# Kernel optimization log

Hardware: AMD Instinct MI355X
Metric: run time of the kernel (lower is better)

Reference implementation:

```python
import jax, jax.numpy as jnp
import numpy as np

N = 10000
F_IN = 512
HID = 256
C = 16
N_POST_ITER = 4


def setup_inputs() -> dict:
    key = jax.random.key(0)
    ks = jax.random.split(key, 10)
    raw_adj = jax.random.uniform(ks[0], (N, N), dtype=jnp.float32) * 0.01
    A = jax.random.uniform(ks[1], (N, N), dtype=jnp.float32)
    normed_adj = A / jnp.sum(A, axis=1, keepdims=True)  # row-sum-one normalized
    features = jax.random.normal(ks[2], (N, F_IN), dtype=jnp.float32)
    labels = jax.random.randint(ks[3], (N,), 0, C)
    y_onehot = jax.nn.one_hot(labels, C, dtype=jnp.float32)
    train_mask = jax.random.randint(ks[4], (N,), 0, 2).astype(jnp.bool_)
    # GCN belief estimator params (glorot-ish scaling)
    W1 = jax.random.normal(ks[5], (F_IN, HID), dtype=jnp.float32) / np.sqrt(F_IN)
    b1 = jnp.zeros((HID,), dtype=jnp.float32)
    W2 = jax.random.normal(ks[6], (HID, C), dtype=jnp.float32) / np.sqrt(HID)
    b2 = jnp.zeros((C,), dtype=jnp.float32)
    # class-compatibility matrix H (initialized, zero-centered as in init_H)
    H = jax.random.normal(ks[7], (C, C), dtype=jnp.float32) * 0.1
    return {"raw_adj": raw_adj, "normed_adj": normed_adj, "features": features,
            "y_onehot": y_onehot, "train_mask": train_mask,
            "W1": W1, "b1": b1, "W2": W2, "b2": b2, "H": H}


def reference(raw_adj, normed_adj, features, y_onehot, train_mask, W1, b1, W2, b2, H):
    num_class = y_onehot.shape[1]
    # 2-layer GCN belief estimator: adj @ (x @ W) + b
    h = jax.nn.relu(normed_adj @ (features @ W1) + b1)          # [N, HID]
    logits = normed_adj @ (h @ W2) + b2                          # [N, C]
    # post_process: iterative compatibility-guided belief propagation
    prior_belief = jax.nn.softmax(logits, axis=1)
    E_hat = prior_belief - 1.0 / num_class
    B_hat = E_hat
    for _ in range(N_POST_ITER):
        B_hat = E_hat + raw_adj @ (B_hat @ H)
    post_belief = B_hat + 1.0 / num_class
    return post_belief
```

## Files before the change

kernel.cpp:

```cpp
#include <hip/hip_runtime.h>

#define NN 10000
#define KP 10048
static constexpr float INV_C = 1.0f / 16.0f;

typedef __attribute__((ext_vector_type(8))) short bf16x8;
typedef __attribute__((ext_vector_type(4))) float f32x4;
typedef unsigned short u16;
typedef unsigned int u32;

__device__ __forceinline__ u16 f2b(float f) {
    union { float f; u32 u; } v; v.f = f;
    u32 r = v.u + 0x7FFFu + ((v.u >> 16) & 1u);
    return (u16)(r >> 16);
}
__device__ __forceinline__ float b2f(u16 b) {
    union { u32 u; float f; } v; v.u = ((u32)b) << 16;
    return v.f;
}

#define AS1(p) ((__attribute__((address_space(1))) void*)(p))
#define AS3(p) ((__attribute__((address_space(3))) void*)(p))
#define NTL4(p)  __builtin_nontemporal_load((const f32x4*)(p))
#define NTL8H(p) __builtin_nontemporal_load((const bf16x8*)(p))

__global__ __launch_bounds__(256)
void cvt_feat(const float* __restrict__ src, u16* __restrict__ dst)
{
    int c = blockIdx.x * 256 + threadIdx.x;
    size_t base = (size_t)c * 8;
    f32x4 a = NTL4(src + base);
    f32x4 b = NTL4(src + base + 4);
    bf16x8 o;
    o[0]=f2b(a[0]); o[1]=f2b(a[1]); o[2]=f2b(a[2]); o[3]=f2b(a[3]);
    o[4]=f2b(b[0]); o[5]=f2b(b[1]); o[6]=f2b(b[2]); o[7]=f2b(b[3]);
    *(bf16x8*)(dst + base) = o;
}

__global__ __launch_bounds__(256)
void w12t(const float* __restrict__ W1, const float* __restrict__ W2,
          float* __restrict__ W1T, u16* __restrict__ W2T)
{
    int bid = blockIdx.x, t = threadIdx.x;
    if (bid < 512) {
        int idx = bid * 256 + t;
        int n = idx >> 9, k = idx & 511;
        W1T[idx] = W1[(size_t)k * 256 + n];
    } else {
        int idx = (bid - 512) * 256 + t;
        if (idx < 4096) {
            int n_ = idx >> 8, k_ = idx & 255;
            W2T[idx] = f2b(W2[(size_t)k_ * 16 + n_]);
        }
    }
}

template<int BIAS, int RELU>
__global__ __launch_bounds__(256)
void gemm_a32_bt16(const float* __restrict__ A, int lda, int M, int Ka,
                   const u16* __restrict__ BT, int ldb, int N, int npad,
                   const float* __restrict__ bias,
                   u16* __restrict__ C, int ldc, int K)
{
    __shared__ u16 Asm[64 * 64];
    __shared__ u16 Bsm[256 * 64];
    const int t = threadIdx.x;
    const int lane = t & 63;
    const int w = t >> 6;
    const int row0 = blockIdx.x * 64;
    const int n0 = blockIdx.y * 256;

    const f32x4 fz = {0.f, 0.f, 0.f, 0.f};
    f32x4 acc[4][4];
#pragma unroll
    for (int i = 0; i < 4; ++i)
#pragma unroll
        for (int j = 0; j < 4; ++j) acc[i][j] = fz;

    const int ar = t >> 2, akq = t & 3;
    int agr = row0 + ar; if (agr > M - 1) agr = M - 1;
    const float* asrc = A + (size_t)agr * lda + akq * 16;
    const int aslot0 = (akq * 2) ^ (ar & 7);
    const int aslot1 = (akq * 2 + 1) ^ (ar & 7);
    const int l8 = lane >> 3, sl = lane & 7;

    for (int k0 = 0; k0 < K; k0 += 64) {
#pragma unroll
        for (int i = 0; i < 8; ++i) {
            int lr = i * 32 + w * 8 + l8;
            int gn = n0 + lr; if (gn > N - 1) gn = N - 1;
            int ss = sl ^ (lr & 7);
            const u16* src = BT + (size_t)gn * ldb + k0 + ss * 8;
            __builtin_amdgcn_global_load_lds(AS1(src), AS3(&Bsm[(i * 32 + w * 8) * 64]),
                                             16, 0, 0);
        }
        bool aval = (k0 + akq * 16) < Ka;
        f32x4 x0, x1, x2, x3;
        if (aval) {
            x0 = *(const f32x4*)(asrc + k0);
            x1 = *(const f32x4*)(asrc + k0 + 4);
            x2 = *(const f32x4*)(asrc + k0 + 8);
            x3 = *(const f32x4*)(asrc + k0 + 12);
        } else {
            x0 = x1 = x2 = x3 = fz;
        }
        bf16x8 p0, p1;
        p0[0]=f2b(x0[0]); p0[1]=f2b(x0[1]); p0[2]=f2b(x0[2]); p0[3]=f2b(x0[3]);
        p0[4]=f2b(x1[0]); p0[5]=f2b(x1[1]); p0[6]=f2b(x1[2]); p0[7]=f2b(x1[3]);
        p1[0]=f2b(x2[0]); p1[1]=f2b(x2[1]); p1[2]=f2b(x2[2]); p1[3]=f2b(x2[3]);
        p1[4]=f2b(x3[0]); p1[5]=f2b(x3[1]); p1[6]=f2b(x3[2]); p1[7]=f2b(x3[3]);
        *(bf16x8*)&Asm[ar * 64 + aslot0 * 8] = p0;
        *(bf16x8*)&Asm[ar * 64 + aslot1 * 8] = p1;
        __syncthreads();
#pragma unroll
        for (int kk = 0; kk < 2; ++kk) {
            bf16x8 afr[4], bfr[4];
#pragma unroll
            for (int mi = 0; mi < 4; ++mi) {
                int r = mi * 16 + (lane & 15);
                int s2 = (kk * 4 + (lane >> 4)) ^ (r & 7);
                afr[mi] = *(const bf16x8*)&Asm[r * 64 + s2 * 8];
            }
#pragma unroll
            for (int ni = 0; ni < 4; ++ni) {
                int nr = w * 64 + ni * 16 + (lane & 15);
                int s2 = (kk * 4 + (lane >> 4)) ^ (nr & 7);
                bfr[ni] = *(const bf16x8*)&Bsm[nr * 64 + s2 * 8];
            }
#pragma unroll
            for (int mi = 0; mi < 4; ++mi)
#pragma unroll
                for (int ni = 0; ni < 4; ++ni)
                    acc[mi][ni] = __builtin_amdgcn_mfma_f32_16x16x32_bf16(
                        afr[mi], bfr[ni], acc[mi][ni], 0, 0, 0);
        }
        __syncthreads();
    }
#pragma unroll
    for (int mi = 0; mi < 4; ++mi) {
        int grb = row0 + mi * 16 + (lane >> 4) * 4;
#pragma unroll
        for (int ni = 0; ni < 4; ++ni) {
            int gc = n0 + w * 64 + ni * 16 + (lane & 15);
            if (gc < npad) {
                float bv = (BIAS && gc < N) ? bias[gc] : 0.f;
#pragma unroll
                for (int rg = 0; rg < 4; ++rg) {
                    int gr = grb + rg;
                    if (gr < M) {
                        float v = acc[mi][ni][rg] + bv;
                        if (RELU) v = fmaxf(v, 0.f);
                        C[(size_t)gr * ldc + gc] = f2b(gc < N ? v : 0.f);
                    }
                }
            }
        }
    }
}

template<int CVT>
__global__ __launch_bounds__(256)
void gemm_na(const float* __restrict__ A, const u16* __restrict__ BT,
             u16* __restrict__ Pws, u16* __restrict__ Acvt)
{
    __shared__ u16 Asm[64 * 64];
    __shared__ u16 Bsm[256 * 64];
    const int t = threadIdx.x;
    const int lane = t & 63;
    const int w = t >> 6;
    const int row0 = blockIdx.x * 64;
    const int s = blockIdx.y;
    const int c0 = (157 * s) >> 3, c1 = (157 * (s + 1)) >> 3;

    const f32x4 fz = {0.f, 0.f, 0.f, 0.f};
    f32x4 acc[4][4];
#pragma unroll
    for (int i = 0; i < 4; ++i)
#pragma unroll
        for (int j = 0; j < 4; ++j) acc[i][j] = fz;

    const int ar = t >> 2, akq = t & 3;
    const int grow = row0 + ar;
    const int agr = grow < NN ? grow : NN - 1;
    const float* asrc = A + (size_t)agr * NN + akq * 16;
    const int aslot0 = (akq * 2) ^ (ar & 7);
    const int aslot1 = (akq * 2 + 1) ^ (ar & 7);
    const int l8 = lane >> 3, sl = lane & 7;

    for (int ck = c0; ck < c1; ++ck) {
        const int k0 = ck * 64;
#pragma unroll
        for (int i = 0; i < 8; ++i) {
            int lr = i * 32 + w * 8 + l8;
            int ss = sl ^ (lr & 7);
            const u16* src = BT + (size_t)lr * KP + k0 + ss * 8;
            __builtin_amdgcn_global_load_lds(AS1(src), AS3(&Bsm[(i * 32 + w * 8) * 64]),
                                             16, 0, 0);
        }
        const int kq0 = k0 + akq * 16;
        bool aval = kq0 < NN;
        f32x4 x0, x1, x2, x3;
        if (aval) {
            x0 = NTL4(asrc + k0);
            x1 = NTL4(asrc + k0 + 4);
            x2 = NTL4(asrc + k0 + 8);
            x3 = NTL4(asrc + k0 + 12);
        } else {
            x0 = x1 = x2 = x3 = fz;
        }
        bf16x8 p0, p1;
        p0[0]=f2b(x0[0]); p0[1]=f2b(x0[1]); p0[2]=f2b(x0[2]); p0[3]=f2b(x0[3]);
        p0[4]=f2b(x1[0]); p0[5]=f2b(x1[1]); p0[6]=f2b(x1[2]); p0[7]=f2b(x1[3]);
        p1[0]=f2b(x2[0]); p1[1]=f2b(x2[1]); p1[2]=f2b(x2[2]); p1[3]=f2b(x2[3]);
        p1[4]=f2b(x3[0]); p1[5]=f2b(x3[1]); p1[6]=f2b(x3[2]); p1[7]=f2b(x3[3]);
        *(bf16x8*)&Asm[ar * 64 + aslot0 * 8] = p0;
        *(bf16x8*)&Asm[ar * 64 + aslot1 * 8] = p1;
        if (CVT && grow < NN) {
            *(bf16x8*)(Acvt + (size_t)grow * KP + kq0) = p0;
            *(bf16x8*)(Acvt + (size_t)grow * KP + kq0 + 8) = p1;
        }
        __syncthreads();
#pragma unroll
        for (int kk = 0; kk < 2; ++kk) {
            bf16x8 afr[4], bfr[4];
#pragma unroll
            for (int mi = 0; mi < 4; ++mi) {
                int r = mi * 16 + (lane & 15);
                int s2 = (kk * 4 + (lane >> 4)) ^ (r & 7);
                afr[mi] = *(const bf16x8*)&Asm[r * 64 + s2 * 8];
            }
#pragma unroll
            for (int ni = 0; ni < 4; ++ni) {
                int nr = w * 64 + ni * 16 + (lane & 15);
                int s2 = (kk * 4 + (lane >> 4)) ^ (nr & 7);
                bfr[ni] = *(const bf16x8*)&Bsm[nr * 64 + s2 * 8];
            }
#pragma unroll
            for (int mi = 0; mi < 4; ++mi)
#pragma unroll
                for (int ni = 0; ni < 4; ++ni)
                    acc[mi][ni] = __builtin_amdgcn_mfma_f32_16x16x32_bf16(
                        afr[mi], bfr[ni], acc[mi][ni], 0, 0, 0);
        }
        __syncthreads();
    }
    u16* outp = Pws + (size_t)s * NN * 256;
#pragma unroll
    for (int mi = 0; mi < 4; ++mi) {
        int grb = row0 + mi * 16 + (lane >> 4) * 4;
#pragma unroll
        for (int ni = 0; ni < 4; ++ni) {
            int gc = w * 64 + ni * 16 + (lane & 15);
#pragma unroll
            for (int rg = 0; rg < 4; ++rg) {
                int gr = grb + rg;
                if (gr < NN)
                    outp[(size_t)gr * 256 + gc] = f2b(acc[mi][ni][rg]);
            }
        }
    }
}

__global__ __launch_bounds__(256)
void reduce_h(const u16* __restrict__ Pws, const float* __restrict__ b1,
              u16* __restrict__ hbf)
{
    int i8 = blockIdx.x * 256 + threadIdx.x;
    size_t base = (size_t)i8 * 8;
    int col = (int)(base & 255);
    float v[8];
#pragma unroll
    for (int j = 0; j < 8; ++j) v[j] = b1[col + j];
#pragma unroll
    for (int s = 0; s < 8; ++s) {
        bf16x8 p = NTL8H(Pws + (size_t)s * NN * 256 + base);
#pragma unroll
        for (int j = 0; j < 8; ++j) v[j] += b2f((u16)p[j]);
    }
    bf16x8 o;
#pragma unroll
    for (int j = 0; j < 8; ++j) o[j] = f2b(fmaxf(v[j], 0.f));
    *(bf16x8*)(hbf + base) = o;
}

template<int AFP32, int CVT, int NTA16>
__global__ __launch_bounds__(256)
void adj16(const void* __restrict__ Av, long lda,
           const u16* __restrict__ BT,
           float* __restrict__ Pout, int nch, int nchf,
           u16* __restrict__ Acvt)
{
    const int t = threadIdx.x, lane = t & 63, w = t >> 6;
    const int s = blockIdx.y;
    const int rowu = blockIdx.x * 64 + w * 16 + (lane & 15);
    const int row = rowu < NN ? rowu : NN - 1;
    const int kq = (lane >> 4) * 8;
    const u16* brow = BT + (size_t)(lane & 15) * KP + kq;
    const float* a32 = (const float*)Av + (size_t)row * lda + kq;
    const u16*  a16 = (const u16*) Av + (size_t)row * lda + kq;
    u16* cvtp = CVT ? (Acvt + (size_t)rowu * KP + kq) : (u16*)0;
    const bool wok = CVT && (rowu < NN);

    int c0 = (nch * s) >> 3, c1 = (nch * (s + 1)) >> 3;
    int c1f = c1 < nchf ? c1 : nchf;
    f32x4 acc = {0.f, 0.f, 0.f, 0.f};
    int kc = c0;
    for (; kc + 4 <= c1f; kc += 4) {
        bf16x8 a[4], b[4];
#pragma unroll
        for (int u = 0; u < 4; ++u) {
            if (AFP32) {
                f32x4 x = NTL4(a32 + (size_t)(kc + u) * 32);
                f32x4 y = NTL4(a32 + (size_t)(kc + u) * 32 + 4);
                bf16x8 r;
                r[0]=f2b(x[0]); r[1]=f2b(x[1]); r[2]=f2b(x[2]); r[3]=f2b(x[3]);
                r[4]=f2b(y[0]); r[5]=f2b(y[1]); r[6]=f2b(y[2]); r[7]=f2b(y[3]);
                a[u] = r;
            } else if (NTA16) {
                a[u] = NTL8H(a16 + (size_t)(kc + u) * 32);
            } else {
                a[u] = *(const bf16x8*)(a16 + (size_t)(kc + u) * 32);
            }
            b[u] = *(const bf16x8*)(brow + (size_t)(kc + u) * 32);
        }
        if (CVT && wok) {
#pragma unroll
            for (int u = 0; u < 4; ++u)
                *(bf16x8*)(cvtp + (size_t)(kc + u) * 32) = a[u];
        }
#pragma unroll
        for (int u = 0; u < 4; ++u)
            acc = __builtin_amdgcn_mfma_f32_16x16x32_bf16(a[u], b[u], acc, 0, 0, 0);
    }
    for (; kc < c1; ++kc) {
        bf16x8 a = bf16x8{0,0,0,0,0,0,0,0};
        if (AFP32) {
            if (kc * 32 + kq < NN) {
                f32x4 x = NTL4(a32 + (size_t)kc * 32);
                f32x4 y = NTL4(a32 + (size_t)kc * 32 + 4);
                a[0]=f2b(x[0]); a[1]=f2b(x[1]); a[2]=f2b(x[2]); a[3]=f2b(x[3]);
                a[4]=f2b(y[0]); a[5]=f2b(y[1]); a[6]=f2b(y[2]); a[7]=f2b(y[3]);
            }
        } else {
            a = *(const bf16x8*)(a16 + (size_t)kc * 32);
        }
        if (CVT && wok)
            *(bf16x8*)(cvtp + (size_t)kc * 32) = a;
        bf16x8 b = *(const bf16x8*)(brow + (size_t)kc * 32);
        acc = __builtin_amdgcn_mfma_f32_16x16x32_bf16(a, b, acc, 0, 0, 0);
    }
    int ob = blockIdx.x * 64 + w * 16 + (lane >> 4) * 4;
#pragma unroll
    for (int rg = 0; rg < 4; ++rg) {
        int orow = ob + rg;
        if (orow < NN)
            Pout[(size_t)s * (NN * 16) + (size_t)orow * 16 + (lane & 15)] = acc[rg];
    }
}

__global__ __launch_bounds__(256)
void hw2_mfma(const u16* __restrict__ h, const u16* __restrict__ W2T,
              u16* __restrict__ outT)
{
    const int t = threadIdx.x, lane = t & 63, w = t >> 6;
    int row = blockIdx.x * 64 + w * 16 + (lane & 15);
    int rowc = row < NN ? row : NN - 1;
    const int kq = (lane >> 4) * 8;
    const u16* arow = h + (size_t)rowc * 256 + kq;
    const u16* brow = W2T + (size_t)(lane & 15) * 256 + kq;
    f32x4 acc = {0.f, 0.f, 0.f, 0.f};
#pragma unroll
    for (int kc = 0; kc < 8; ++kc) {
        bf16x8 a = *(const bf16x8*)(arow + kc * 32);
        bf16x8 b = *(const bf16x8*)(brow + kc * 32);
        acc = __builtin_amdgcn_mfma_f32_16x16x32_bf16(a, b, acc, 0, 0, 0);
    }
    int ob = blockIdx.x * 64 + w * 16 + (lane >> 4) * 4;
    int col = lane & 15;
#pragma unroll
    for (int rg = 0; rg < 4; ++rg) {
        int r = ob + rg;
        outT[(size_t)col * KP + r] = f2b(r < NN ? acc[rg] : 0.f);
    }
}

__global__ __launch_bounds__(256)
void softmax_e_h2(const float* __restrict__ P, const float* __restrict__ b2,
                  const float* __restrict__ H, float* __restrict__ E,
                  u16* __restrict__ bhT)
{
    __shared__ float Hs[256];
    const int t = threadIdx.x;
    Hs[t] = H[t];
    __syncthreads();
    const int l = t & 63, w = t >> 6;
    const int g = l >> 2, sub = l & 3;
    const int row = blockIdx.x * 64 + w * 16 + g;
    const bool valid = row < NN;
    float acc[16];
#pragma unroll
    for (int k = 0; k < 16; ++k) acc[k] = 0.f;
    if (valid) {
        const float* p0 = P + (size_t)(sub * 2) * (NN * 16) + (size_t)row * 16;
        const float* p1 = p0 + (size_t)NN * 16;
#pragma unroll
        for (int q = 0; q < 4; ++q) {
            f32x4 a = *(const f32x4*)(p0 + q * 4);
            f32x4 c = *(const f32x4*)(p1 + q * 4);
#pragma unroll
            for (int j = 0; j < 4; ++j) acc[q * 4 + j] = a[j] + c[j];
        }
        if (sub == 0) {
#pragma unroll
            for (int k = 0; k < 16; ++k) acc[k] += b2[k];
        }
    }
#pragma unroll
    for (int m = 1; m <= 2; m <<= 1)
#pragma unroll
        for (int k = 0; k < 16; ++k) acc[k] += __shfl_xor(acc[k], m, 4);
    float e[16];
    if (valid) {
        float mx = acc[0];
#pragma unroll
        for (int k = 1; k < 16; ++k) mx = fmaxf(mx, acc[k]);
        float ssum = 0.f;
#pragma unroll
        for (int k = 0; k < 16; ++k) { e[k] = __expf(acc[k] - mx); ssum += e[k]; }
        float inv = 1.f / ssum;
#pragma unroll
        for (int k = 0; k < 16; ++k) e[k] = e[k] * inv - INV_C;
        f32x4 eq = {e[sub*4+0], e[sub*4+1], e[sub*4+2], e[sub*4+3]};
        *(f32x4*)(E + (size_t)row * 16 + sub * 4) = eq;
    } else {
#pragma unroll
        for (int k = 0; k < 16; ++k) e[k] = 0.f;
    }
    float o[4] = {0.f, 0.f, 0.f, 0.f};
#pragma unroll
    for (int m2 = 0; m2 < 16; ++m2) {
        float x = e[m2];
#pragma unroll
        for (int j = 0; j < 4; ++j) o[j] += x * Hs[m2 * 16 + sub * 4 + j];
    }
#pragma unroll
    for (int j = 0; j < 4; ++j)
        bhT[(size_t)(sub * 4 + j) * KP + row] = f2b(o[j]);
}

template<int LAST>
__global__ __launch_bounds__(256)
void combine_bmm2(const float* __restrict__ E, const float* __restrict__ P,
                  const float* __restrict__ H, u16* __restrict__ bhT,
                  float* __restrict__ out)
{
    __shared__ float Hs[256];
    const int t = threadIdx.x;
    Hs[t] = H[t];
    __syncthreads();
    const int l = t & 63, w = t >> 6;
    const int g = l >> 2, sub = l & 3;
    const int row = blockIdx.x * 64 + w * 16 + g;
    const bool valid = row < NN;
    float acc[16];
#pragma unroll
    for (int k = 0; k < 16; ++k) acc[k] = 0.f;
    if (valid) {
        const float* p0 = P + (size_t)(sub * 2) * (NN * 16) + (size_t)row * 16;
        const float* p1 = p0 + (size_t)NN * 16;
#pragma unroll
        for (int q = 0; q < 4; ++q) {
            f32x4 a = *(const f32x4*)(p0 + q * 4);
            f32x4 c = *(const f32x4*)(p1 + q * 4);
#pragma unroll
            for (int j = 0; j < 4; ++j) acc[q * 4 + j] = a[j] + c[j];
        }
        if (sub == 0) {
            const float* ep = E + (size_t)row * 16;
#pragma unroll
            for (int k = 0; k < 16; ++k) acc[k] += ep[k];
        }
    }
#pragma unroll
    for (int m = 1; m <= 2; m <<= 1)
#pragma unroll
        for (int k = 0; k < 16; ++k) acc[k] += __shfl_xor(acc[k], m, 4);
    if (LAST) {
        if (valid) {
            f32x4 oq = {acc[sub*4+0] + INV_C, acc[sub*4+1] + INV_C,
                        acc[sub*4+2] + INV_C, acc[sub*4+3] + INV_C};
            *(f32x4*)(out + (size_t)row * 16 + sub * 4) = oq;
        }
    } else {
        if (!valid) {
#pragma unroll
            for (int k = 0; k < 16; ++k) acc[k] = 0.f;
        }
        float o[4] = {0.f, 0.f, 0.f, 0.f};
#pragma unroll
        for (int m2 = 0; m2 < 16; ++m2) {
            float x = acc[m2];
#pragma unroll
            for (int j = 0; j < 4; ++j) o[j] += x * Hs[m2 * 16 + sub * 4 + j];
        }
#pragma unroll
        for (int j = 0; j < 4; ++j)
            bhT[(size_t)(sub * 4 + j) * KP + row] = f2b(o[j]);
    }
}

extern "C" void kernel_launch(void* const* d_in, const int* in_sizes, int n_in,
                              void* d_out, int out_size, void* d_ws, size_t ws_size,
                              hipStream_t stream)
{
    const float* raw_adj    = (const float*)d_in[0];
    const float* normed_adj = (const float*)d_in[1];
    const float* features   = (const float*)d_in[2];
    const float* W1 = (const float*)d_in[5];
    const float* b1 = (const float*)d_in[6];
    const float* W2 = (const float*)d_in[7];
    const float* b2 = (const float*)d_in[8];
    const float* H  = (const float*)d_in[9];
    float* out = (float*)d_out;

    char* ws = (char*)d_ws;
    u16*   featbf = (u16*)  (ws + 0);
    float* P      = (float*)(ws + 0);
    float* E      = (float*)(ws + 5120000);
    float* W1T    = (float*)(ws + 10240000);
    u16*   W2T    = (u16*)  (ws + 10764288);
    u16*   XWT    = (u16*)  (ws + 10772480);
    u16*   hbf    = (u16*)  (ws + 15917056);
    u16*   hw2T   = (u16*)  (ws + 21037056);
    u16*   bhT    = (u16*)  (ws + 21358592);
    const bool full = ws_size >= (size_t)263600128;
    const bool mid  = ws_size >= (size_t)222640128;
    const bool low  = ws_size >= (size_t)62640128;
    u16* An_bf = (u16*)(ws + 21680128);
    u16* ArBf  = (u16*)(ws + 21680128);
    u16* Pws   = (u16*)(ws + (full ? 222640128 : 21680128));

    cvt_feat<<<2500, 256, 0, stream>>>(features, featbf);
    w12t<<<528, 256, 0, stream>>>(W1, W2, W1T, W2T);

    gemm_a32_bt16<0, 0><<<dim3(4, 40), 256, 0, stream>>>(
        W1T, 512, 256, 512, featbf, 512, NN, KP, nullptr, XWT, KP, 512);

    if (low) {
        if (full)
            gemm_na<1><<<dim3(157, 8), 256, 0, stream>>>(normed_adj, XWT, Pws, An_bf);
        else
            gemm_na<0><<<dim3(157, 8), 256, 0, stream>>>(normed_adj, XWT, Pws, nullptr);
        reduce_h<<<1250, 256, 0, stream>>>(Pws, b1, hbf);
    } else {
        gemm_a32_bt16<1, 1><<<dim3(157, 1), 256, 0, stream>>>(
            normed_adj, NN, NN, NN, XWT, KP, 256, 256, b1, hbf, 256, KP);
    }

    hw2_mfma<<<157, 256, 0, stream>>>(hbf, W2T, hw2T);

    if (full)
        adj16<0, 0, 1><<<dim3(157, 8), 256, 0, stream>>>(
            (const void*)An_bf, KP, hw2T, P, 314, 314, nullptr);
    else
        adj16<1, 0, 0><<<dim3(157, 8), 256, 0, stream>>>(
            (const void*)normed_adj, NN, hw2T, P, 313, 312, nullptr);

    softmax_e_h2<<<157, 256, 0, stream>>>(P, b2, H, E, bhT);

    for (int it = 0; it < 4; ++it) {
        if (mid) {
            if (it == 0)
                adj16<1, 1, 0><<<dim3(157, 8), 256, 0, stream>>>(
                    (const void*)raw_adj, NN, bhT, P, 314, 312, ArBf);
            else
                adj16<0, 0, 0><<<dim3(157, 8), 256, 0, stream>>>(
                    (const void*)ArBf, KP, bhT, P, 314, 314, nullptr);
        } else {
            adj16<1, 0, 0><<<dim3(157, 8), 256, 0, stream>>>(
                (const void*)raw_adj, NN, bhT, P, 313, 312, nullptr);
        }
        if (it == 3)
            combine_bmm2<1><<<157, 256, 0, stream>>>(E, P, H, nullptr, out);
        else
            combine_bmm2<0><<<157, 256, 0, stream>>>(E, P, H, bhT, nullptr);
    }
}
```

Measured before the change: 670.0 us.

## Split normed_adj GEMM into 16 K-slices, drop nontemporal loads, dual accumulators

Doubles the K-split of the first adjacency GEMM from 8 to 16 slices, giving more blocks, and has reduce_h sum 16 partial buffers. The workspace thresholds grow to fit the larger partial buffer. All nontemporal loads become ordinary loads. The bf16 conversion now uses the library intrinsic, the A loads are issued before the B LDS loads, and adj16 splits its MFMA chain across two accumulators to shorten the dependency chain. The trade-offs are more partial-sum traffic, and the larger workspace requirement may push execution onto a slower fallback path.

New measurement: 605.3 us. -9.7%, faster.

```diff
diff --git a/kernel.cpp b/kernel.cpp
--- a/kernel.cpp
+++ b/kernel.cpp
@@ -1,4 +1,5 @@
 #include <hip/hip_runtime.h>
+#include <hip/hip_bf16.h>
 
 #define NN 10000
 #define KP 10048
@@ -10,31 +11,30 @@
 typedef unsigned int u32;
 
 __device__ __forceinline__ u16 f2b(float f) {
-    union { float f; u32 u; } v; v.f = f;
-    u32 r = v.u + 0x7FFFu + ((v.u >> 16) & 1u);
-    return (u16)(r >> 16);
+    return __builtin_bit_cast(u16, __float2bfloat16(f));
 }
 __device__ __forceinline__ float b2f(u16 b) {
     union { u32 u; float f; } v; v.u = ((u32)b) << 16;
     return v.f;
 }
-
-#define AS1(p) ((__attribute__((address_space(1))) void*)(p))
-#define AS3(p) ((__attribute__((address_space(3))) void*)(p))
-#define NTL4(p)  __builtin_nontemporal_load((const f32x4*)(p))
-#define NTL8H(p) __builtin_nontemporal_load((const bf16x8*)(p))
-
-__global__ __launch_bounds__(256)
-void cvt_feat(const float* __restrict__ src, u16* __restrict__ dst)
-{
-    int c = blockIdx.x * 256 + threadIdx.x;
-    size_t base = (size_t)c * 8;
-    f32x4 a = NTL4(src + base);
-    f32x4 b = NTL4(src + base + 4);
+__device__ __forceinline__ bf16x8 pack8(f32x4 a, f32x4 b) {
     bf16x8 o;
     o[0]=f2b(a[0]); o[1]=f2b(a[1]); o[2]=f2b(a[2]); o[3]=f2b(a[3]);
     o[4]=f2b(b[0]); o[5]=f2b(b[1]); o[6]=f2b(b[2]); o[7]=f2b(b[3]);
-    *(bf16x8*)(dst + base) = o;
+    return o;
+}
+
+#define AS1(p) ((__attribute__((address_space(1))) void*)(p))
+#define AS3(p) ((__attribute__((address_space(3))) void*)(p))
+
+__global__ __launch_bounds__(256)
+void cvt_feat(const float* __restrict__ src, u16* __restrict__ dst)
+{
+    int c = blockIdx.x * 256 + threadIdx.x;
+    size_t base = (size_t)c * 8;
+    f32x4 a = *(const f32x4*)(src + base);
+    f32x4 b = *(const f32x4*)(src + base + 4);
+    *(bf16x8*)(dst + base) = pack8(a, b);
 }
 
 __global__ __launch_bounds__(256)
@@ -85,15 +85,6 @@
     const int l8 = lane >> 3, sl = lane & 7;
 
     for (int k0 = 0; k0 < K; k0 += 64) {
-#pragma unroll
-        for (int i = 0; i < 8; ++i) {
-            int lr = i * 32 + w * 8 + l8;
-            int gn = n0 + lr; if (gn > N - 1) gn = N - 1;
-            int ss = sl ^ (lr & 7);
-            const u16* src = BT + (size_t)gn * ldb + k0 + ss * 8;
-            __builtin_amdgcn_global_load_lds(AS1(src), AS3(&Bsm[(i * 32 + w * 8) * 64]),
-                                             16, 0, 0);
-        }
         bool aval = (k0 + akq * 16) < Ka;
         f32x4 x0, x1, x2, x3;
         if (aval) {
@@ -104,13 +95,17 @@
         } else {
             x0 = x1 = x2 = x3 = fz;
         }
-        bf16x8 p0, p1;
-        p0[0]=f2b(x0[0]); p0[1]=f2b(x0[1]); p0[2]=f2b(x0[2]); p0[3]=f2b(x0[3]);
-        p0[4]=f2b(x1[0]); p0[5]=f2b(x1[1]); p0[6]=f2b(x1[2]); p0[7]=f2b(x1[3]);
-        p1[0]=f2b(x2[0]); p1[1]=f2b(x2[1]); p1[2]=f2b(x2[2]); p1[3]=f2b(x2[3]);
-        p1[4]=f2b(x3[0]); p1[5]=f2b(x3[1]); p1[6]=f2b(x3[2]); p1[7]=f2b(x3[3]);
-        *(bf16x8*)&Asm[ar * 64 + aslot0 * 8] = p0;
-        *(bf16x8*)&Asm[ar * 64 + aslot1 * 8] = p1;
+#pragma unroll
+        for (int i = 0; i < 8; ++i) {
+            int lr = i * 32 + w * 8 + l8;
+            int gn = n0 + lr; if (gn > N - 1) gn = N - 1;
+            int ss = sl ^ (lr & 7);
+            const u16* src = BT + (size_t)gn * ldb + k0 + ss * 8;
+            __builtin_amdgcn_global_load_lds(AS1(src), AS3(&Bsm[(i * 32 + w * 8) * 64]),
+                                             16, 0, 0);
+        }
+        *(bf16x8*)&Asm[ar * 64 + aslot0 * 8] = pack8(x0, x1);
+        *(bf16x8*)&Asm[ar * 64 + aslot1 * 8] = pack8(x2, x3);
         __syncthreads();
 #pragma unroll
         for (int kk = 0; kk < 2; ++kk) {
@@ -170,7 +165,7 @@
     const int w = t >> 6;
     const int row0 = blockIdx.x * 64;
     const int s = blockIdx.y;
-    const int c0 = (157 * s) >> 3, c1 = (157 * (s + 1)) >> 3;
+    const int c0 = (157 * s) >> 4, c1 = (157 * (s + 1)) >> 4;
 
     const f32x4 fz = {0.f, 0.f, 0.f, 0.f};
     f32x4 acc[4][4];
@@ -189,6 +184,17 @@
 
     for (int ck = c0; ck < c1; ++ck) {
         const int k0 = ck * 64;
+        const int kq0 = k0 + akq * 16;
+        bool aval = kq0 < NN;
+        f32x4 x0, x1, x2, x3;
+        if (aval) {
+            x0 = *(const f32x4*)(asrc + k0);
+            x1 = *(const f32x4*)(asrc + k0 + 4);
+            x2 = *(const f32x4*)(asrc + k0 + 8);
+            x3 = *(const f32x4*)(asrc + k0 + 12);
+        } else {
+            x0 = x1 = x2 = x3 = fz;
+        }
 #pragma unroll
         for (int i = 0; i < 8; ++i) {
             int lr = i * 32 + w * 8 + l8;
@@ -197,22 +203,7 @@
             __builtin_amdgcn_global_load_lds(AS1(src), AS3(&Bsm[(i * 32 + w * 8) * 64]),
                                              16, 0, 0);
         }
-        const int kq0 = k0 + akq * 16;
-        bool aval = kq0 < NN;
-        f32x4 x0, x1, x2, x3;
-        if (aval) {
-            x0 = NTL4(asrc + k0);
-            x1 = NTL4(asrc + k0 + 4);
-            x2 = NTL4(asrc + k0 + 8);
-            x3 = NTL4(asrc + k0 + 12);
-        } else {
-            x0 = x1 = x2 = x3 = fz;
-        }
-        bf16x8 p0, p1;
-        p0[0]=f2b(x0[0]); p0[1]=f2b(x0[1]); p0[2]=f2b(x0[2]); p0[3]=f2b(x0[3]);
-        p0[4]=f2b(x1[0]); p0[5]=f2b(x1[1]); p0[6]=f2b(x1[2]); p0[7]=f2b(x1[3]);
-        p1[0]=f2b(x2[0]); p1[1]=f2b(x2[1]); p1[2]=f2b(x2[2]); p1[3]=f2b(x2[3]);
-        p1[4]=f2b(x3[0]); p1[5]=f2b(x3[1]); p1[6]=f2b(x3[2]); p1[7]=f2b(x3[3]);
+        bf16x8 p0 = pack8(x0, x1), p1 = pack8(x2, x3);
         *(bf16x8*)&Asm[ar * 64 + aslot0 * 8] = p0;
         *(bf16x8*)&Asm[ar * 64 + aslot1 * 8] = p1;
         if (CVT && grow < NN) {
@@ -272,8 +263,8 @@
 #pragma unroll
     for (int j = 0; j < 8; ++j) v[j] = b1[col + j];
 #pragma unroll
-    for (int s = 0; s < 8; ++s) {
-        bf16x8 p = NTL8H(Pws + (size_t)s * NN * 256 + base);
+    for (int s = 0; s < 16; ++s) {
+        bf16x8 p = *(const bf16x8*)(Pws + (size_t)s * NN * 256 + base);
 #pragma unroll
         for (int j = 0; j < 8; ++j) v[j] += b2f((u16)p[j]);
     }
@@ -283,7 +274,7 @@
     *(bf16x8*)(hbf + base) = o;
 }
 
-template<int AFP32, int CVT, int NTA16>
+template<int AFP32, int CVT>
 __global__ __launch_bounds__(256)
 void adj16(const void* __restrict__ Av, long lda,
            const u16* __restrict__ BT,
@@ -303,21 +294,17 @@
 
     int c0 = (nch * s) >> 3, c1 = (nch * (s + 1)) >> 3;
     int c1f = c1 < nchf ? c1 : nchf;
-    f32x4 acc = {0.f, 0.f, 0.f, 0.f};
+    f32x4 acc0 = {0.f, 0.f, 0.f, 0.f};
+    f32x4 acc1 = {0.f, 0.f, 0.f, 0.f};
     int kc = c0;
     for (; kc + 4 <= c1f; kc += 4) {
         bf16x8 a[4], b[4];
 #pragma unroll
         for (int u = 0; u < 4; ++u) {
             if (AFP32) {
-                f32x4 x = NTL4(a32 + (size_t)(kc + u) * 32);
-                f32x4 y = NTL4(a32 + (size_t)(kc + u) * 32 + 4);
-                bf16x8 r;
-                r[0]=f2b(x[0]); r[1]=f2b(x[1]); r[2]=f2b(x[2]); r[3]=f2b(x[3]);
-                r[4]=f2b(y[0]); r[5]=f2b(y[1]); r[6]=f2b(y[2]); r[7]=f2b(y[3]);
-                a[u] = r;
-            } else if (NTA16) {
-                a[u] = NTL8H(a16 + (size_t)(kc + u) * 32);
+                f32x4 x = *(const f32x4*)(a32 + (size_t)(kc + u) * 32);
+                f32x4 y = *(const f32x4*)(a32 + (size_t)(kc + u) * 32 + 4);
+                a[u] = pack8(x, y);
             } else {
                 a[u] = *(const bf16x8*)(a16 + (size_t)(kc + u) * 32);
             }
@@ -328,18 +315,18 @@
             for (int u = 0; u < 4; ++u)
                 *(bf16x8*)(cvtp + (size_t)(kc + u) * 32) = a[u];
         }
-#pragma unroll
-        for (int u = 0; u < 4; ++u)
-            acc = __builtin_amdgcn_mfma_f32_16x16x32_bf16(a[u], b[u], acc, 0, 0, 0);
+        acc0 = __builtin_amdgcn_mfma_f32_16x16x32_bf16(a[0], b[0], acc0, 0, 0, 0);
+        acc1 = __builtin_amdgcn_mfma_f32_16x16x32_bf16(a[1], b[1], acc1, 0, 0, 0);
+        acc0 = __builtin_amdgcn_mfma_f32_16x16x32_bf16(a[2], b[2], acc0, 0, 0, 0);
+        acc1 = __builtin_amdgcn_mfma_f32_16x16x32_bf16(a[3], b[3], acc1, 0, 0, 0);
     }
     for (; kc < c1; ++kc) {
         bf16x8 a = bf16x8{0,0,0,0,0,0,0,0};
         if (AFP32) {
             if (kc * 32 + kq < NN) {
-                f32x4 x = NTL4(a32 + (size_t)kc * 32);
-                f32x4 y = NTL4(a32 + (size_t)kc * 32 + 4);
-                a[0]=f2b(x[0]); a[1]=f2b(x[1]); a[2]=f2b(x[2]); a[3]=f2b(x[3]);
-                a[4]=f2b(y[0]); a[5]=f2b(y[1]); a[6]=f2b(y[2]); a[7]=f2b(y[3]);
+                f32x4 x = *(const f32x4*)(a32 + (size_t)kc * 32);
+                f32x4 y = *(const f32x4*)(a32 + (size_t)kc * 32 + 4);
+                a = pack8(x, y);
             }
         } else {
             a = *(const bf16x8*)(a16 + (size_t)kc * 32);
@@ -347,14 +334,15 @@
         if (CVT && wok)
             *(bf16x8*)(cvtp + (size_t)kc * 32) = a;
         bf16x8 b = *(const bf16x8*)(brow + (size_t)kc * 32);
-        acc = __builtin_amdgcn_mfma_f32_16x16x32_bf16(a, b, acc, 0, 0, 0);
+        acc0 = __builtin_amdgcn_mfma_f32_16x16x32_bf16(a, b, acc0, 0, 0, 0);
     }
     int ob = blockIdx.x * 64 + w * 16 + (lane >> 4) * 4;
 #pragma unroll
     for (int rg = 0; rg < 4; ++rg) {
         int orow = ob + rg;
         if (orow < NN)
-            Pout[(size_t)s * (NN * 16) + (size_t)orow * 16 + (lane & 15)] = acc[rg];
+            Pout[(size_t)s * (NN * 16) + (size_t)orow * 16 + (lane & 15)] =
+                acc0[rg] + acc1[rg];
     }
 }
 
@@ -533,9 +521,9 @@
     u16*   hbf    = (u16*)  (ws + 15917056);
     u16*   hw2T   = (u16*)  (ws + 21037056);
     u16*   bhT    = (u16*)  (ws + 21358592);
-    const bool full = ws_size >= (size_t)263600128;
+    const bool full = ws_size >= (size_t)304560128;
     const bool mid  = ws_size >= (size_t)222640128;
-    const bool low  = ws_size >= (size_t)62640128;
+    const bool low  = ws_size >= (size_t)103600128;
     u16* An_bf = (u16*)(ws + 21680128);
     u16* ArBf  = (u16*)(ws + 21680128);
     u16* Pws   = (u16*)(ws + (full ? 222640128 : 21680128));
@@ -548,9 +536,9 @@
 
     if (low) {
         if (full)
-            gemm_na<1><<<dim3(157, 8), 256, 0, stream>>>(normed_adj, XWT, Pws, An_bf);
+            gemm_na<1><<<dim3(157, 16), 256, 0, stream>>>(normed_adj, XWT, Pws, An_bf);
         else
-            gemm_na<0><<<dim3(157, 8), 256, 0, stream>>>(normed_adj, XWT, Pws, nullptr);
+            gemm_na<0><<<dim3(157, 16), 256, 0, stream>>>(normed_adj, XWT, Pws, nullptr);
         reduce_h<<<1250, 256, 0, stream>>>(Pws, b1, hbf);
     } else {
         gemm_a32_bt16<1, 1><<<dim3(157, 1), 256, 0, stream>>>(
@@ -560,10 +548,10 @@
     hw2_mfma<<<157, 256, 0, stream>>>(hbf, W2T, hw2T);
 
     if (full)
-        adj16<0, 0, 1><<<dim3(157, 8), 256, 0, stream>>>(
+        adj16<0, 0><<<dim3(157, 8), 256, 0, stream>>>(
             (const void*)An_bf, KP, hw2T, P, 314, 314, nullptr);
     else
-        adj16<1, 0, 0><<<dim3(157, 8), 256, 0, stream>>>(
+        adj16<1, 0><<<dim3(157, 8), 256, 0, stream>>>(
             (const void*)normed_adj, NN, hw2T, P, 313, 312, nullptr);
 
     softmax_e_h2<<<157, 256, 0, stream>>>(P, b2, H, E, bhT);
@@ -571,13 +559,13 @@
     for (int it = 0; it < 4; ++it) {
         if (mid) {
             if (it == 0)
-                adj16<1, 1, 0><<<dim3(157, 8), 256, 0, stream>>>(
+                adj16<1, 1><<<dim3(157, 8), 256, 0, stream>>>(
                     (const void*)raw_adj, NN, bhT, P, 314, 312, ArBf);
             else
-                adj16<0, 0, 0><<<dim3(157, 8), 256, 0, stream>>>(
+                adj16<0, 0><<<dim3(157, 8), 256, 0, stream>>>(
                     (const void*)ArBf, KP, bhT, P, 314, 314, nullptr);
         } else {
-            adj16<1, 0, 0><<<dim3(157, 8), 256, 0, stream>>>(
+            adj16<1, 0><<<dim3(157, 8), 256, 0, stream>>>(
                 (const void*)raw_adj, NN, bhT, P, 313, 312, nullptr);
         }
         if (it == 3)
```
